# Optimization experiments

Hardware: AMD Instinct MI355X
Metric: run time of the kernel (lower is better)

Reference implementation:

```python
import jax, jax.numpy as jnp
import numpy as np

LN_EPS = 1e-5
N_HEADS = 8
N_POINTS = 4


def layer_norm(x, g, b):
    m = x.mean(-1, keepdims=True)
    v = ((x - m) ** 2).mean(-1, keepdims=True)
    return (x - m) / jnp.sqrt(v + LN_EPS) * g + b


def msda(query, ref, src, ts, lsi, mask, Wv, bv, Wo, bo, Wa, ba, Wp, bp):
    # 1D multi-scale deformable attention (temporal, as in PDVC/SAGA-DVC).
    B, Lq, D = query.shape
    Lin = src.shape[0] * 0 + src.shape[1]
    ts_np = np.asarray(ts)
    lsi_np = np.asarray(lsi)
    L = ts_np.shape[0]
    H, P = N_HEADS, N_POINTS
    Dh = D // H
    value = src @ Wv + bv
    value = jnp.where(mask[..., None], 0.0, value).reshape(B, Lin, H, Dh)
    off = (query @ Wo + bo).reshape(B, Lq, H, L, P)
    aw = jax.nn.softmax((query @ Wa + ba).reshape(B, Lq, H, L * P), axis=-1)
    aw = aw.reshape(B, Lq, H, L, P)
    norm = jnp.asarray(ts_np).astype(query.dtype)  # (L,)
    # sampling locations in normalized [0,1] coords: (B,Lq,H,L,P)
    loc = ref[:, :, None, :, None, 0] + off / norm[None, None, None, :, None]
    b_idx = jnp.arange(B)[:, None, None, None]
    h_idx = jnp.arange(H)[None, None, :, None]
    out = jnp.zeros((B, Lq, H, Dh), query.dtype)
    for l in range(L):  # small fixed number of levels
        T = int(ts_np[l]); s = int(lsi_np[l])
        v = value[:, s:s + T]  # (B,T,H,Dh)
        # grid_sample align_corners=False: pixel pos = loc*T - 0.5
        pos = loc[:, :, :, l, :] * T - 0.5  # (B,Lq,H,P)
        x0 = jnp.floor(pos)
        w1 = (pos - x0)[..., None]
        x0i = x0.astype(jnp.int32)

        def gather(xi):
            valid = ((xi >= 0) & (xi < T))[..., None].astype(v.dtype)
            xc = jnp.clip(xi, 0, T - 1)
            return v[b_idx, xc, h_idx] * valid  # (B,Lq,H,P,Dh), zeros pad

        samp = gather(x0i) * (1.0 - w1) + gather(x0i + 1) * w1
        out = out + (samp * aw[:, :, :, l, :, None]).sum(axis=3)
    out = out.reshape(B, Lq, D) @ Wp + bp
    return out, loc, aw


def ffn(x, W1, b1, W2, b2, ln2_g, ln2_b):
    h = jax.nn.relu(x @ W1 + b1) @ W2 + b2
    return layer_norm(x + h, ln2_g, ln2_b)


def setup_inputs() -> dict:
    key = jax.random.key(0)
    ks = jax.random.split(key, 24)
    B, S, D = 8, 3840, 256
    L = 4
    ts = jnp.array([2048, 1024, 512, 256], dtype=jnp.int32)
    lsi = jnp.array([0, 2048, 3072, 3584], dtype=jnp.int32)
    HP = N_HEADS * L * N_POINTS  # 128
    sc = 0.02
    inp = {
        'video_src': jax.random.normal(ks[0], (B, S, D), jnp.float32),
        'audio_src': jax.random.normal(ks[1], (B, S, D), jnp.float32),
        'video_pos': jax.random.normal(ks[2], (B, S, D), jnp.float32),
        'audio_pos': jax.random.normal(ks[3], (B, S, D), jnp.float32),
        'video_ref': jax.random.uniform(ks[4], (B, S, L, 1), jnp.float32),
        'audio_ref': jax.random.uniform(ks[5], (B, S, L, 1), jnp.float32),
        'video_ts': ts, 'video_lsi': lsi,
        'video_mask': jnp.zeros((B, S), jnp.bool_),
        'audio_ts': ts, 'audio_lsi': lsi,
        'audio_mask': jnp.zeros((B, S), jnp.bool_),
        'Wv': jax.random.normal(ks[6], (D, D)) * sc, 'bv': jnp.zeros((D,)),
        'Wo': jax.random.normal(ks[7], (D, HP)) * sc, 'bo': jnp.zeros((HP,)),
        'Wa': jax.random.normal(ks[8], (D, HP)) * sc, 'ba': jnp.zeros((HP,)),
        'Wp': jax.random.normal(ks[9], (D, D)) * sc, 'bp': jnp.zeros((D,)),
        'ln1_g': jnp.ones((D,)), 'ln1_b': jnp.zeros((D,)),
        'W1': jax.random.normal(ks[10], (D, 1024)) * sc, 'b1': jnp.zeros((1024,)),
        'W2': jax.random.normal(ks[11], (1024, D)) * sc, 'b2': jnp.zeros((D,)),
        'ln2_g': jnp.ones((D,)), 'ln2_b': jnp.zeros((D,)),
    }
    return inp


def reference(video_src, audio_src, video_pos, audio_pos, video_ref, audio_ref,
              video_ts, video_lsi, video_mask, audio_ts, audio_lsi, audio_mask,
              Wv, bv, Wo, bo, Wa, ba, Wp, bp, ln1_g, ln1_b,
              W1, b1, W2, b2, ln2_g, ln2_b):
    attn = (Wv, bv, Wo, bo, Wa, ba, Wp, bp)
    # modality self-attention (dropout = identity at eval)
    v2, _, _ = msda(video_src + video_pos, video_ref, video_src,
                    video_ts, video_lsi, video_mask, *attn)
    video = layer_norm(video_src + v2, ln1_g, ln1_b)
    a2, _, _ = msda(audio_src + audio_pos, audio_ref, audio_src,
                    audio_ts, audio_lsi, audio_mask, *attn)
    audio = layer_norm(audio_src + a2, ln1_g, ln1_b)
    # cross-modal deformable attention
    vaa, a_loc, a_aw = msda(audio, audio_ref, video,
                            video_ts, video_lsi, video_mask, *attn)
    aav, v_loc, v_aw = msda(video, video_ref, audio,
                            audio_ts, audio_lsi, audio_mask, *attn)
    vaa = ffn(vaa, W1, b1, W2, b2, ln2_g, ln2_b)
    aav = ffn(aav, W1, b1, W2, b2, ln2_g, ln2_b)
    return (aav, vaa, v_loc, v_aw, a_loc, a_aw)
```

## Files before the change

### kernel.cpp

```cpp
#include <hip/hip_runtime.h>
#include <hip/hip_bf16.h>
#include <cstdint>

#define BB 8
#define SS 3840
#define RR (BB*SS)
#define NHALF ((size_t)RR * 256)

typedef short s16x8 __attribute__((ext_vector_type(8)));
typedef float f32x4 __attribute__((ext_vector_type(4)));

__device__ __forceinline__ ushort f2bf(float f) {
    uint32_t u = __builtin_bit_cast(uint32_t, f);
    u += 0x7FFFu + ((u >> 16) & 1u);
    return (ushort)(u >> 16);
}
__device__ __forceinline__ float bf2f(ushort h) {
    return __builtin_bit_cast(float, (uint32_t)h << 16);
}

#define GLDS16(gp, lp) __builtin_amdgcn_global_load_lds( \
    (const __attribute__((address_space(1))) uint32_t*)(gp), \
    (__attribute__((address_space(3))) uint32_t*)(lp), 16, 0, 0)

__global__ __launch_bounds__(256) void wtrans_all(
    const float* __restrict__ Wv, const float* __restrict__ Wo,
    const float* __restrict__ Wa, const float* __restrict__ Wp,
    const float* __restrict__ W1, const float* __restrict__ W2,
    const float* __restrict__ bo, const float* __restrict__ ba,
    ushort* __restrict__ Wvt, ushort* __restrict__ Woat, ushort* __restrict__ Wpt,
    ushort* __restrict__ W1t, ushort* __restrict__ W2t, float* __restrict__ boa)
{
    int e = blockIdx.x * 256 + threadIdx.x;
    if (e < 65536)       { int k = e >> 8, n = e & 255;  Wvt[n * 256 + k] = f2bf(Wv[e]); }
    else if (e < 98304)  { int i = e - 65536;  int k = i >> 7, n = i & 127;  Woat[n * 256 + k] = f2bf(Wo[i]); }
    else if (e < 131072) { int i = e - 98304;  int k = i >> 7, n = i & 127;  Woat[(n + 128) * 256 + k] = f2bf(Wa[i]); }
    else if (e < 196608) { int i = e - 131072; int k = i >> 8, n = i & 255;  Wpt[n * 256 + k] = f2bf(Wp[i]); }
    else if (e < 458752) { int i = e - 196608; int k = i >> 10, n = i & 1023; W1t[n * 256 + k] = f2bf(W1[i]); }
    else if (e < 720896) { int i = e - 458752; int k = i >> 8, n = i & 255;  W2t[(size_t)n * 1024 + k] = f2bf(W2[i]); }
    else if (e < 721152) { int t = e - 720896; boa[t] = (t < 128) ? bo[t] : ba[t - 128]; }
}

__global__ __launch_bounds__(256) void pack2_cat(
    const float* __restrict__ vs, const float* __restrict__ as_,
    const float* __restrict__ vp, const float* __restrict__ ap,
    ushort* __restrict__ sb, ushort* __restrict__ qb)
{
    const int n4 = (int)(NHALF / 4);
    int i = blockIdx.x * 256 + threadIdx.x;
    int j = (i < n4) ? i : i - n4;
    const float4* s4 = (const float4*)((i < n4) ? vs : as_);
    const float4* p4 = (const float4*)((i < n4) ? vp : ap);
    float4 a = s4[j];
    float4 b = p4[j];
    ushort4 u, v;
    u.x = f2bf(a.x); u.y = f2bf(a.y); u.z = f2bf(a.z); u.w = f2bf(a.w);
    v.x = f2bf(a.x + b.x); v.y = f2bf(a.y + b.y); v.z = f2bf(a.z + b.z); v.w = f2bf(a.w + b.w);
    ((ushort4*)sb)[i] = u;
    ((ushort4*)qb)[i] = v;
}

__global__ __launch_bounds__(256) void gemm_fused(
    const ushort* __restrict__ Av0, const ushort* __restrict__ Av1,
    const ushort* __restrict__ Ao0, const ushort* __restrict__ Ao1,
    const ushort* __restrict__ WvT, const ushort* __restrict__ WoT,
    const float* __restrict__ bv, const float* __restrict__ boa,
    ushort* __restrict__ val_out,
    float* __restrict__ loc0, float* __restrict__ loc1,
    float* __restrict__ aw0, float* __restrict__ aw1,
    const float* __restrict__ ref0, const float* __restrict__ ref1,
    const int* __restrict__ ts0, const int* __restrict__ ts1,
    const unsigned char* __restrict__ mask0, const unsigned char* __restrict__ mask1)
{
    __shared__ ushort As[128 * 64];
    __shared__ ushort Bs[128 * 64];
    const int tid = threadIdx.x;
    const int lane = tid & 63;
    const int wid = tid >> 6;
    const int wr = wid >> 1, wc = wid & 1;
    const int job = blockIdx.y >> 1;
    const int bn = (blockIdx.y & 1) << 7;
    const int bm = blockIdx.x << 7;
    const int half = bm >= RR;
    const int bmL = half ? bm - RR : bm;
    const int l15 = lane & 15;
    const int l4 = lane >> 4;

    const ushort* A = job ? (half ? Ao1 : Ao0) : (half ? Av1 : Av0);
    const ushort* Wt = job ? WoT : WvT;
    A += (size_t)bmL * 256;

    f32x4 acc[4][4] = {};

    for (int k0 = 0; k0 < 256; k0 += 64) {
        #pragma unroll
        for (int r = 0; r < 4; ++r) {
            int base = r * 256 + (wid << 6);
            int idx = base + lane;
            int row = idx >> 3, sl = idx & 7;
            int ch = sl ^ (row & 7);
            GLDS16(&A[(size_t)row * 256 + k0 + ch * 8], &As[base << 3]);
        }
        #pragma unroll
        for (int r = 0; r < 4; ++r) {
            int base = r * 256 + (wid << 6);
            int idx = base + lane;
            int col = idx >> 3, sl = idx & 7;
            int ch = sl ^ (col & 7);
            GLDS16(&Wt[(size_t)(bn + col) * 256 + k0 + ch * 8], &Bs[base << 3]);
        }
        __syncthreads();
        #pragma unroll
        for (int ks = 0; ks < 2; ++ks) {
            s16x8 af[4], bf[4];
            const int k16 = ks * 4 + l4;
            #pragma unroll
            for (int m = 0; m < 4; ++m) {
                int row = (wr << 6) + (m << 4) + l15;
                af[m] = *(const s16x8*)&As[(row << 6) + ((k16 ^ (row & 7)) << 3)];
            }
            #pragma unroll
            for (int n = 0; n < 4; ++n) {
                int col = (wc << 6) + (n << 4) + l15;
                bf[n] = *(const s16x8*)&Bs[(col << 6) + ((k16 ^ (col & 7)) << 3)];
            }
            #pragma unroll
            for (int m = 0; m < 4; ++m)
                #pragma unroll
                for (int n = 0; n < 4; ++n)
                    acc[m][n] = __builtin_amdgcn_mfma_f32_16x16x32_bf16(af[m], bf[n], acc[m][n], 0, 0, 0);
        }
        __syncthreads();
    }

    const int l4r = l4 << 2;
    if (job == 0) {
        const unsigned char* mk = half ? mask1 : mask0;
        ushort* vo = val_out + (size_t)half * NHALF;
        #pragma unroll
        for (int m = 0; m < 4; ++m) {
            #pragma unroll
            for (int r = 0; r < 4; ++r) {
                const int rowL = bmL + (wr << 6) + (m << 4) + l4r + r;
                const int b = rowL / SS;
                const int s = rowL - b * SS;
                const float mz = mk[rowL] ? 0.f : 1.f;
                const size_t rb = ((size_t)(b * 8) * SS + s) * 32;
                #pragma unroll
                for (int n = 0; n < 4; ++n) {
                    const int col = bn + (wc << 6) + (n << 4) + l15;
                    const int h = col >> 5, d = col & 31;
                    vo[rb + (size_t)h * (SS * 32) + d] = f2bf((acc[m][n][r] + bv[col]) * mz);
                }
            }
        }
    } else if (bn == 0) {
        const float* rf = half ? ref1 : ref0;
        const int* tsp = half ? ts1 : ts0;
        const int l = l15 >> 2;
        const float T = (float)tsp[l];
        float* lo = half ? loc1 : loc0;
        #pragma unroll
        for (int m = 0; m < 4; ++m) {
            #pragma unroll
            for (int r = 0; r < 4; ++r) {
                const int rowL = bmL + (wr << 6) + (m << 4) + l4r + r;
                const float refv = rf[(size_t)rowL * 4 + l];
                #pragma unroll
                for (int n = 0; n < 4; ++n) {
                    const int cc = (wc << 6) + (n << 4) + l15;
                    lo[(size_t)rowL * 128 + cc] = refv + (acc[m][n][r] + boa[cc]) / T;
                }
            }
        }
    } else {
        float* ao = half ? aw1 : aw0;
        #pragma unroll
        for (int m = 0; m < 4; ++m) {
            #pragma unroll
            for (int r = 0; r < 4; ++r) {
                const int rowL = bmL + (wr << 6) + (m << 4) + l4r + r;
                #pragma unroll
                for (int n = 0; n < 4; ++n) {
                    const int cc = (wc << 6) + (n << 4) + l15;
                    float c = acc[m][n][r] + boa[128 + cc];
                    float mx = c;
                    #pragma unroll
                    for (int o = 1; o < 16; o <<= 1) mx = fmaxf(mx, __shfl_xor(mx, o));
                    float e = __expf(c - mx);
                    float sm = e;
                    #pragma unroll
                    for (int o = 1; o < 16; o <<= 1) sm += __shfl_xor(sm, o);
                    ao[(size_t)rowL * 128 + cc] = e / sm;
                }
            }
        }
    }
}

template<int RELU, int WF, int WB>
__global__ __launch_bounds__(256) void gemm_mfma(
    const ushort* __restrict__ A, const ushort* __restrict__ Wt,
    const float* __restrict__ bias,
    float* __restrict__ C, ushort* __restrict__ Cb, int N, int K)
{
    __shared__ ushort As[128 * 64];
    __shared__ ushort Bs[128 * 64];
    const int tid = threadIdx.x;
    const int lane = tid & 63;
    const int wid = tid >> 6;
    const int wr = wid >> 1, wc = wid & 1;
    const int bm = blockIdx.x << 7;
    const int bn = blockIdx.y << 7;
    const int l15 = lane & 15;
    const int l4 = lane >> 4;

    f32x4 acc[4][4] = {};

    for (int k0 = 0; k0 < K; k0 += 64) {
        #pragma unroll
        for (int r = 0; r < 4; ++r) {
            int base = r * 256 + (wid << 6);
            int idx = base + lane;
            int row = idx >> 3, sl = idx & 7;
            int ch = sl ^ (row & 7);
            GLDS16(&A[(size_t)(bm + row) * K + k0 + ch * 8], &As[base << 3]);
        }
        #pragma unroll
        for (int r = 0; r < 4; ++r) {
            int base = r * 256 + (wid << 6);
            int idx = base + lane;
            int col = idx >> 3, sl = idx & 7;
            int ch = sl ^ (col & 7);
            GLDS16(&Wt[(size_t)(bn + col) * K + k0 + ch * 8], &Bs[base << 3]);
        }
        __syncthreads();
        #pragma unroll
        for (int ks = 0; ks < 2; ++ks) {
            s16x8 af[4], bf[4];
            const int k16 = ks * 4 + l4;
            #pragma unroll
            for (int m = 0; m < 4; ++m) {
                int row = (wr << 6) + (m << 4) + l15;
                af[m] = *(const s16x8*)&As[(row << 6) + ((k16 ^ (row & 7)) << 3)];
            }
            #pragma unroll
            for (int n = 0; n < 4; ++n) {
                int col = (wc << 6) + (n << 4) + l15;
                bf[n] = *(const s16x8*)&Bs[(col << 6) + ((k16 ^ (col & 7)) << 3)];
            }
            #pragma unroll
            for (int m = 0; m < 4; ++m)
                #pragma unroll
                for (int n = 0; n < 4; ++n)
                    acc[m][n] = __builtin_amdgcn_mfma_f32_16x16x32_bf16(af[m], bf[n], acc[m][n], 0, 0, 0);
        }
        __syncthreads();
    }

    #pragma unroll
    for (int m = 0; m < 4; ++m) {
        #pragma unroll
        for (int r = 0; r < 4; ++r) {
            const int row = bm + (wr << 6) + (m << 4) + (l4 << 2) + r;
            #pragma unroll
            for (int n = 0; n < 4; ++n) {
                const int col = bn + (wc << 6) + (n << 4) + l15;
                float c = acc[m][n][r] + bias[col];
                if (RELU) c = fmaxf(c, 0.f);
                if (WF) C[(size_t)row * N + col] = c;
                if (WB) Cb[(size_t)row * N + col] = f2bf(c);
            }
        }
    }
}

struct Desc { float wa, wb; int oa, ob; };

__global__ __launch_bounds__(256) void msda_sample(
    const ushort* __restrict__ value,
    const float* __restrict__ l0, const float* __restrict__ l1,
    const float* __restrict__ a0, const float* __restrict__ a1,
    const int* __restrict__ ts0, const int* __restrict__ lsi0,
    const int* __restrict__ ts1, const int* __restrict__ lsi1,
    ushort* __restrict__ out)
{
    __shared__ Desc ds[512];
    const int tid = threadIdx.x;
    const int row0 = blockIdx.x << 2;
    const int half = row0 >= RR;
    const int rowL0 = half ? row0 - RR : row0;
    const float* loc = half ? l1 : l0;
    const float* aw  = half ? a1 : a0;
    const int* ts  = half ? ts1 : ts0;
    const int* lsi = half ? lsi1 : lsi0;
    const ushort* val = value + (size_t)half * NHALF;

    #pragma unroll
    for (int d = tid; d < 512; d += 256) {
        const int rl = d >> 7;
        const int rem = d & 127;
        const int l = (rem >> 2) & 3;
        const int h = rem >> 4;
        const int rowL = rowL0 + rl;
        const float lc = loc[(size_t)rowL * 128 + rem];
        const float w  = aw[(size_t)rowL * 128 + rem];
        const int T = ts[l];
        const int s0 = lsi[l];
        const int b = rowL / SS;
        const float pos = lc * (float)T - 0.5f;
        const float x0 = floorf(pos);
        const float w1 = pos - x0;
        const int i0 = (int)x0;
        const int i1 = i0 + 1;
        const int base = (b * 8 + h) * SS + s0;
        Desc e;
        e.wa = (i0 >= 0 && i0 < T) ? w * (1.f - w1) : 0.f;
        e.wb = (i1 >= 0 && i1 < T) ? w * w1 : 0.f;
        const int ia = min(max(i0, 0), T - 1);
        const int ib = min(max(i1, 0), T - 1);
        e.oa = (base + ia) << 5;
        e.ob = (base + ib) << 5;
        ds[d] = e;
    }
    __syncthreads();

    const int rl = tid >> 6;
    const int h  = (tid >> 3) & 7;
    const int cq = tid & 7;
    const ushort* vb = val + cq * 4;
    const Desc* dd = &ds[rl * 128 + h * 16];

    f32x4 acc0 = {}, acc1 = {};
    #pragma unroll
    for (int lp = 0; lp < 16; lp += 2) {
        const Desc e0 = dd[lp];
        const Desc e1 = dd[lp + 1];
        const uint2 A0 = *(const uint2*)(vb + e0.oa);
        const uint2 B0 = *(const uint2*)(vb + e0.ob);
        const uint2 A1 = *(const uint2*)(vb + e1.oa);
        const uint2 B1 = *(const uint2*)(vb + e1.ob);
        #pragma unroll
        for (int c = 0; c < 2; ++c) {
            const uint32_t ua = (c ? A0.y : A0.x), ub = (c ? B0.y : B0.x);
            const uint32_t va = (c ? A1.y : A1.x), vw = (c ? B1.y : B1.x);
            acc0[2*c+0] = fmaf(e0.wa, __builtin_bit_cast(float, ua << 16), acc0[2*c+0]);
            acc0[2*c+1] = fmaf(e0.wa, __builtin_bit_cast(float, ua & 0xFFFF0000u), acc0[2*c+1]);
            acc0[2*c+0] = fmaf(e0.wb, __builtin_bit_cast(float, ub << 16), acc0[2*c+0]);
            acc0[2*c+1] = fmaf(e0.wb, __builtin_bit_cast(float, ub & 0xFFFF0000u), acc0[2*c+1]);
            acc1[2*c+0] = fmaf(e1.wa, __builtin_bit_cast(float, va << 16), acc1[2*c+0]);
            acc1[2*c+1] = fmaf(e1.wa, __builtin_bit_cast(float, va & 0xFFFF0000u), acc1[2*c+1]);
            acc1[2*c+0] = fmaf(e1.wb, __builtin_bit_cast(float, vw << 16), acc1[2*c+0]);
            acc1[2*c+1] = fmaf(e1.wb, __builtin_bit_cast(float, vw & 0xFFFF0000u), acc1[2*c+1]);
        }
    }
    ushort4 o;
    o.x = f2bf(acc0[0] + acc1[0]);
    o.y = f2bf(acc0[1] + acc1[1]);
    o.z = f2bf(acc0[2] + acc1[2]);
    o.w = f2bf(acc0[3] + acc1[3]);
    *(ushort4*)&out[(size_t)(row0 + rl) * 256 + h * 32 + cq * 4] = o;
}

template<int MODE>
__global__ __launch_bounds__(256) void add_ln4(
    const float* __restrict__ a0, const float* __restrict__ a1,
    const ushort* __restrict__ pb, const float* __restrict__ bf,
    const float* __restrict__ g, const float* __restrict__ be,
    ushort* __restrict__ ob, float* __restrict__ of0, float* __restrict__ of1)
{
    const int tid = threadIdx.x;
    const int row = (blockIdx.x << 2) + (tid >> 6);
    const int lane = tid & 63;
    const int half = row >= RR;
    const int rowL = half ? row - RR : row;

    ushort4 pv = ((const ushort4*)(pb + (size_t)row * 256))[lane];
    float px = bf2f(pv.x), py = bf2f(pv.y), pz = bf2f(pv.z), pw = bf2f(pv.w);
    float4 x;
    if (MODE == 0) {
        const float* a = half ? a1 : a0;
        float4 av = ((const float4*)(a + (size_t)rowL * 256))[lane];
        x.x = av.x + px; x.y = av.y + py; x.z = av.z + pz; x.w = av.w + pw;
    } else {
        float4 fv = ((const float4*)(bf + (size_t)row * 256))[lane];
        x.x = fv.x + px; x.y = fv.y + py; x.z = fv.z + pz; x.w = fv.w + pw;
    }
    float s1 = x.x + x.y + x.z + x.w;
    float s2 = x.x * x.x + x.y * x.y + x.z * x.z + x.w * x.w;
    #pragma unroll
    for (int o = 32; o > 0; o >>= 1) {
        s1 += __shfl_xor(s1, o);
        s2 += __shfl_xor(s2, o);
    }
    const float m = s1 * (1.f / 256.f);
    float v = s2 * (1.f / 256.f) - m * m;
    v = fmaxf(v, 0.f);
    const float r = rsqrtf(v + 1e-5f);
    float4 g4 = ((const float4*)g)[lane];
    float4 b4 = ((const float4*)be)[lane];
    float4 y;
    y.x = (x.x - m) * r * g4.x + b4.x;
    y.y = (x.y - m) * r * g4.y + b4.y;
    y.z = (x.z - m) * r * g4.z + b4.z;
    y.w = (x.w - m) * r * g4.w + b4.w;
    if (MODE == 0) {
        ushort4 o;
        o.x = f2bf(y.x); o.y = f2bf(y.y); o.z = f2bf(y.z); o.w = f2bf(y.w);
        ((ushort4*)(ob + (size_t)row * 256))[lane] = o;
    } else {
        ((float4*)((half ? of1 : of0) + (size_t)rowL * 256))[lane] = y;
    }
}

extern "C" void kernel_launch(void* const* d_in, const int* in_sizes, int n_in,
                              void* d_out, int out_size, void* d_ws, size_t ws_size,
                              hipStream_t stream) {
    const float* video_src = (const float*)d_in[0];
    const float* audio_src = (const float*)d_in[1];
    const float* video_pos = (const float*)d_in[2];
    const float* audio_pos = (const float*)d_in[3];
    const float* video_ref = (const float*)d_in[4];
    const float* audio_ref = (const float*)d_in[5];
    const int*   video_ts  = (const int*)d_in[6];
    const int*   video_lsi = (const int*)d_in[7];
    const unsigned char* video_mask = (const unsigned char*)d_in[8];
    const int*   audio_ts  = (const int*)d_in[9];
    const int*   audio_lsi = (const int*)d_in[10];
    const unsigned char* audio_mask = (const unsigned char*)d_in[11];
    const float* Wv = (const float*)d_in[12];
    const float* bv = (const float*)d_in[13];
    const float* Wo = (const float*)d_in[14];
    const float* bo = (const float*)d_in[15];
    const float* Wa = (const float*)d_in[16];
    const float* ba = (const float*)d_in[17];
    const float* Wp = (const float*)d_in[18];
    const float* bp = (const float*)d_in[19];
    const float* ln1_g = (const float*)d_in[20];
    const float* ln1_b = (const float*)d_in[21];
    const float* W1 = (const float*)d_in[22];
    const float* b1 = (const float*)d_in[23];
    const float* W2 = (const float*)d_in[24];
    const float* b2 = (const float*)d_in[25];
    const float* ln2_g = (const float*)d_in[26];
    const float* ln2_b = (const float*)d_in[27];

    float* out = (float*)d_out;
    const size_t n = NHALF;
    float* out_aav  = out;
    float* out_vaa  = out + n;
    float* out_vloc = out + 2 * n;
    float* out_vaw  = out + 2 * n + n / 2;
    float* out_aloc = out + 3 * n;
    float* out_aaw  = out + 3 * n + n / 2;

    const size_t UB = NHALF * 2;
    char* base = (char*)d_ws;
    ushort* src_cat   = (ushort*)(base + 0 * UB);
    ushort* q_cat     = (ushort*)(base + 2 * UB);
    float*  loc_tmp   = (float*) (base + 4 * UB);
    float*  aw_tmp    = (float*) (base + 6 * UB);
    ushort* hid       = (ushort*)(base + 0 * UB);
    ushort* value_cat = (ushort*)(base + 8 * UB);
    ushort* samp_cat  = (ushort*)(base + 10 * UB);
    float*  ffnout    = (float*) (base + 8 * UB);
    ushort* vb_cat    = (ushort*)(base + 12 * UB);
    ushort* proj_b34  = (ushort*)(base + 12 * UB);
    ushort* proj_b12  = (ushort*)(base + 4 * UB);
    ushort* Wvt  = (ushort*)(base + 14 * UB);
    ushort* Woat = Wvt + 65536;
    ushort* Wpt  = Woat + 65536;
    ushort* W1t  = Wpt + 65536;
    ushort* W2t  = W1t + 262144;
    float*  boa  = (float*)(W2t + 262144);

    wtrans_all<<<2817, 256, 0, stream>>>(Wv, Wo, Wa, Wp, W1, W2, bo, ba,
                                         Wvt, Woat, Wpt, W1t, W2t, boa);
    pack2_cat<<<15360, 256, 0, stream>>>(video_src, audio_src, video_pos, audio_pos,
                                         src_cat, q_cat);

    gemm_fused<<<dim3(480, 4), 256, 0, stream>>>(
        src_cat, src_cat + NHALF, q_cat, q_cat + NHALF,
        Wvt, Woat, bv, boa, value_cat,
        loc_tmp, loc_tmp + (size_t)RR * 128, aw_tmp, aw_tmp + (size_t)RR * 128,
        video_ref, audio_ref, video_ts, audio_ts, video_mask, audio_mask);
    msda_sample<<<15360, 256, 0, stream>>>(
        value_cat, loc_tmp, loc_tmp + (size_t)RR * 128, aw_tmp, aw_tmp + (size_t)RR * 128,
        video_ts, video_lsi, audio_ts, audio_lsi, samp_cat);
    gemm_mfma<0,0,1><<<dim3(480, 2), 256, 0, stream>>>(samp_cat, Wpt, bp, nullptr, proj_b12, 256, 256);
    add_ln4<0><<<15360, 256, 0, stream>>>(video_src, audio_src, proj_b12, nullptr,
                                          ln1_g, ln1_b, vb_cat, nullptr, nullptr);

    gemm_fused<<<dim3(480, 4), 256, 0, stream>>>(
        vb_cat, vb_cat + NHALF,
        vb_cat + NHALF, vb_cat,
        Wvt, Woat, bv, boa, value_cat,
        out_aloc, out_vloc, out_aaw, out_vaw,
        audio_ref, video_ref, video_ts, audio_ts, video_mask, audio_mask);
    msda_sample<<<15360, 256, 0, stream>>>(
        value_cat, out_aloc, out_vloc, out_aaw, out_vaw,
        video_ts, video_lsi, audio_ts, audio_lsi, samp_cat);
    gemm_mfma<0,0,1><<<dim3(480, 2), 256, 0, stream>>>(samp_cat, Wpt, bp, nullptr, proj_b34, 256, 256);
    gemm_mfma<1,0,1><<<dim3(480, 8), 256, 0, stream>>>(proj_b34, W1t, b1, nullptr, hid, 1024, 256);
    gemm_mfma<0,1,0><<<dim3(480, 2), 256, 0, stream>>>(hid, W2t, b2, ffnout, nullptr, 256, 1024);
    add_ln4<1><<<15360, 256, 0, stream>>>(nullptr, nullptr, proj_b34, ffnout,
                                          ln2_g, ln2_b, nullptr, out_vaa, out_aav);
}
```

Before: 489.5 us.

## Fuse residual add and LayerNorm into 128x256-tile GEMM epilogue

Replaces the 128x128 GEMM with a 512-thread 128x256-tile variant whose N tile covers a full 256-wide row, so the residual add and LayerNorm can run in the epilogue through a shared-memory cross-wave row reduction. This removes both add_ln4 kernels and the fp32/bf16 intermediate round-trips through global memory (proj_b12, ffnout). The FFN GEMMs also use the larger tile, which means fewer blocks and more shared memory and registers per block, possibly lowering occupancy.

Result: faster. 434.5 us (-11.2%).

```diff
diff --git a/kernel.cpp b/kernel.cpp
--- a/kernel.cpp
+++ b/kernel.cpp
@@ -198,20 +198,29 @@
     }
 }
 
-template<int RELU, int WF, int WB>
-__global__ __launch_bounds__(256) void gemm_mfma(
+template<int EPI>
+__global__ __launch_bounds__(512) void gemm256(
     const ushort* __restrict__ A, const ushort* __restrict__ Wt,
-    const float* __restrict__ bias,
-    float* __restrict__ C, ushort* __restrict__ Cb, int N, int K)
+    const float* __restrict__ bias, int N, int K,
+    ushort* __restrict__ outb,
+    const float* __restrict__ res0, const float* __restrict__ res1,
+    const ushort* __restrict__ resb,
+    const float* __restrict__ g, const float* __restrict__ be,
+    float* __restrict__ of0, float* __restrict__ of1)
 {
     __shared__ ushort As[128 * 64];
-    __shared__ ushort Bs[128 * 64];
+    __shared__ ushort Bs[256 * 64];
+    __shared__ float redS[128][4];
+    __shared__ float redQ[128][4];
+    __shared__ float redM[128];
+    __shared__ float redR[128];
+
     const int tid = threadIdx.x;
     const int lane = tid & 63;
     const int wid = tid >> 6;
-    const int wr = wid >> 1, wc = wid & 1;
+    const int wr = wid >> 2, wc = wid & 3;
     const int bm = blockIdx.x << 7;
-    const int bn = blockIdx.y << 7;
+    const int bn = blockIdx.y << 8;
     const int l15 = lane & 15;
     const int l4 = lane >> 4;
 
@@ -219,8 +228,8 @@
 
     for (int k0 = 0; k0 < K; k0 += 64) {
         #pragma unroll
-        for (int r = 0; r < 4; ++r) {
-            int base = r * 256 + (wid << 6);
+        for (int r = 0; r < 2; ++r) {
+            int base = r * 512 + (wid << 6);
             int idx = base + lane;
             int row = idx >> 3, sl = idx & 7;
             int ch = sl ^ (row & 7);
@@ -228,7 +237,7 @@
         }
         #pragma unroll
         for (int r = 0; r < 4; ++r) {
-            int base = r * 256 + (wid << 6);
+            int base = r * 512 + (wid << 6);
             int idx = base + lane;
             int col = idx >> 3, sl = idx & 7;
             int ch = sl ^ (col & 7);
@@ -258,18 +267,83 @@
         __syncthreads();
     }
 
+    const int half = bm >= RR;
+    const int bmL = half ? bm - RR : bm;
+
+    if (EPI == 0 || EPI == 2) {
+        #pragma unroll
+        for (int m = 0; m < 4; ++m) {
+            #pragma unroll
+            for (int r = 0; r < 4; ++r) {
+                const int row = bm + (wr << 6) + (m << 4) + (l4 << 2) + r;
+                #pragma unroll
+                for (int n = 0; n < 4; ++n) {
+                    const int col = bn + (wc << 6) + (n << 4) + l15;
+                    float c = acc[m][n][r] + bias[col];
+                    if (EPI == 2) c = fmaxf(c, 0.f);
+                    outb[(size_t)row * N + col] = f2bf(c);
+                }
+            }
+        }
+        return;
+    }
+
     #pragma unroll
     for (int m = 0; m < 4; ++m) {
         #pragma unroll
         for (int r = 0; r < 4; ++r) {
-            const int row = bm + (wr << 6) + (m << 4) + (l4 << 2) + r;
+            const int rowb = (wr << 6) + (m << 4) + (l4 << 2) + r;
+            float s1 = 0.f, s2 = 0.f;
             #pragma unroll
             for (int n = 0; n < 4; ++n) {
-                const int col = bn + (wc << 6) + (n << 4) + l15;
-                float c = acc[m][n][r] + bias[col];
-                if (RELU) c = fmaxf(c, 0.f);
-                if (WF) C[(size_t)row * N + col] = c;
-                if (WB) Cb[(size_t)row * N + col] = f2bf(c);
+                const int col = (wc << 6) + (n << 4) + l15;
+                float x = acc[m][n][r] + bias[col];
+                if (EPI == 1) {
+                    const float* res = half ? res1 : res0;
+                    x += res[(size_t)(bmL + rowb) * 256 + col];
+                } else {
+                    x += bf2f(resb[(size_t)(bm + rowb) * 256 + col]);
+                }
+                acc[m][n][r] = x;
+                s1 += x;
+                s2 += x * x;
+            }
+            #pragma unroll
+            for (int o = 1; o < 16; o <<= 1) {
+                s1 += __shfl_xor(s1, o);
+                s2 += __shfl_xor(s2, o);
+            }
+            if (l15 == 0) { redS[rowb][wc] = s1; redQ[rowb][wc] = s2; }
+        }
+    }
+    __syncthreads();
+    if (tid < 128) {
+        const float S1 = redS[tid][0] + redS[tid][1] + redS[tid][2] + redS[tid][3];
+        const float S2 = redQ[tid][0] + redQ[tid][1] + redQ[tid][2] + redQ[tid][3];
+        const float mu = S1 * (1.f / 256.f);
+        float var = S2 * (1.f / 256.f) - mu * mu;
+        var = fmaxf(var, 0.f);
+        redM[tid] = mu;
+        redR[tid] = rsqrtf(var + 1e-5f);
+    }
+    __syncthreads();
+    #pragma unroll
+    for (int m = 0; m < 4; ++m) {
+        #pragma unroll
+        for (int r = 0; r < 4; ++r) {
+            const int rowb = (wr << 6) + (m << 4) + (l4 << 2) + r;
+            const float mu = redM[rowb];
+            const float rs = redR[rowb];
+            #pragma unroll
+            for (int n = 0; n < 4; ++n) {
+                const int col = (wc << 6) + (n << 4) + l15;
+                const float y = (acc[m][n][r] - mu) * rs * g[col] + be[col];
+                if (EPI == 1) {
+                    outb[(size_t)(bm + rowb) * 256 + col] = f2bf(y);
+                } else {
+                    float* of = half ? of1 : of0;
+                    of[(size_t)(bmL + rowb) * 256 + col] = y;
+                }
             }
         }
     }
@@ -360,57 +434,6 @@
     o.z = f2bf(acc0[2] + acc1[2]);
     o.w = f2bf(acc0[3] + acc1[3]);
     *(ushort4*)&out[(size_t)(row0 + rl) * 256 + h * 32 + cq * 4] = o;
-}
-
-template<int MODE>
-__global__ __launch_bounds__(256) void add_ln4(
-    const float* __restrict__ a0, const float* __restrict__ a1,
-    const ushort* __restrict__ pb, const float* __restrict__ bf,
-    const float* __restrict__ g, const float* __restrict__ be,
-    ushort* __restrict__ ob, float* __restrict__ of0, float* __restrict__ of1)
-{
-    const int tid = threadIdx.x;
-    const int row = (blockIdx.x << 2) + (tid >> 6);
-    const int lane = tid & 63;
-    const int half = row >= RR;
-    const int rowL = half ? row - RR : row;
-
-    ushort4 pv = ((const ushort4*)(pb + (size_t)row * 256))[lane];
-    float px = bf2f(pv.x), py = bf2f(pv.y), pz = bf2f(pv.z), pw = bf2f(pv.w);
-    float4 x;
-    if (MODE == 0) {
-        const float* a = half ? a1 : a0;
-        float4 av = ((const float4*)(a + (size_t)rowL * 256))[lane];
-        x.x = av.x + px; x.y = av.y + py; x.z = av.z + pz; x.w = av.w + pw;
-    } else {
-        float4 fv = ((const float4*)(bf + (size_t)row * 256))[lane];
-        x.x = fv.x + px; x.y = fv.y + py; x.z = fv.z + pz; x.w = fv.w + pw;
-    }
-    float s1 = x.x + x.y + x.z + x.w;
-    float s2 = x.x * x.x + x.y * x.y + x.z * x.z + x.w * x.w;
-    #pragma unroll
-    for (int o = 32; o > 0; o >>= 1) {
-        s1 += __shfl_xor(s1, o);
-        s2 += __shfl_xor(s2, o);
-    }
-    const float m = s1 * (1.f / 256.f);
-    float v = s2 * (1.f / 256.f) - m * m;
-    v = fmaxf(v, 0.f);
-    const float r = rsqrtf(v + 1e-5f);
-    float4 g4 = ((const float4*)g)[lane];
-    float4 b4 = ((const float4*)be)[lane];
-    float4 y;
-    y.x = (x.x - m) * r * g4.x + b4.x;
-    y.y = (x.y - m) * r * g4.y + b4.y;
-    y.z = (x.z - m) * r * g4.z + b4.z;
-    y.w = (x.w - m) * r * g4.w + b4.w;
-    if (MODE == 0) {
-        ushort4 o;
-        o.x = f2bf(y.x); o.y = f2bf(y.y); o.z = f2bf(y.z); o.w = f2bf(y.w);
-        ((ushort4*)(ob + (size_t)row * 256))[lane] = o;
-    } else {
-        ((float4*)((half ? of1 : of0) + (size_t)rowL * 256))[lane] = y;
-    }
 }
 
 extern "C" void kernel_launch(void* const* d_in, const int* in_sizes, int n_in,
@@ -463,10 +486,8 @@
     ushort* hid       = (ushort*)(base + 0 * UB);
     ushort* value_cat = (ushort*)(base + 8 * UB);
     ushort* samp_cat  = (ushort*)(base + 10 * UB);
-    float*  ffnout    = (float*) (base + 8 * UB);
     ushort* vb_cat    = (ushort*)(base + 12 * UB);
     ushort* proj_b34  = (ushort*)(base + 12 * UB);
-    ushort* proj_b12  = (ushort*)(base + 4 * UB);
     ushort* Wvt  = (ushort*)(base + 14 * UB);
     ushort* Woat = Wvt + 65536;
     ushort* Wpt  = Woat + 65536;
@@ -487,9 +508,9 @@
     msda_sample<<<15360, 256, 0, stream>>>(
         value_cat, loc_tmp, loc_tmp + (size_t)RR * 128, aw_tmp, aw_tmp + (size_t)RR * 128,
         video_ts, video_lsi, audio_ts, audio_lsi, samp_cat);
-    gemm_mfma<0,0,1><<<dim3(480, 2), 256, 0, stream>>>(samp_cat, Wpt, bp, nullptr, proj_b12, 256, 256);
-    add_ln4<0><<<15360, 256, 0, stream>>>(video_src, audio_src, proj_b12, nullptr,
-                                          ln1_g, ln1_b, vb_cat, nullptr, nullptr);
+    gemm256<1><<<dim3(480, 1), 512, 0, stream>>>(
+        samp_cat, Wpt, bp, 256, 256, vb_cat,
+        video_src, audio_src, nullptr, ln1_g, ln1_b, nullptr, nullptr);
 
     gemm_fused<<<dim3(480, 4), 256, 0, stream>>>(
         vb_cat, vb_cat + NHALF,
@@ -500,9 +521,13 @@
     msda_sample<<<15360, 256, 0, stream>>>(
         value_cat, out_aloc, out_vloc, out_aaw, out_vaw,
         video_ts, video_lsi, audio_ts, audio_lsi, samp_cat);
-    gemm_mfma<0,0,1><<<dim3(480, 2), 256, 0, stream>>>(samp_cat, Wpt, bp, nullptr, proj_b34, 256, 256);
-    gemm_mfma<1,0,1><<<dim3(480, 8), 256, 0, stream>>>(proj_b34, W1t, b1, nullptr, hid, 1024, 256);
-    gemm_mfma<0,1,0><<<dim3(480, 2), 256, 0, stream>>>(hid, W2t, b2, ffnout, nullptr, 256, 1024);
-    add_ln4<1><<<15360, 256, 0, stream>>>(nullptr, nullptr, proj_b34, ffnout,
-                                          ln2_g, ln2_b, nullptr, out_vaa, out_aav);
-}
+    gemm256<0><<<dim3(480, 1), 512, 0, stream>>>(
+        samp_cat, Wpt, bp, 256, 256, proj_b34,
+        nullptr, nullptr, nullptr, nullptr, nullptr, nullptr, nullptr);
+    gemm256<2><<<dim3(480, 4), 512, 0, stream>>>(
+        proj_b34, W1t, b1, 1024, 256, hid,
+        nullptr, nullptr, nullptr, nullptr, nullptr, nullptr, nullptr);
+    gemm256<3><<<dim3(480, 1), 512, 0, stream>>>(
+        hid, W2t, b2, 256, 1024, nullptr,
+        nullptr, nullptr, proj_b34, ln2_g, ln2_b, out_vaa, out_aav);
+}
```
